# Kernel optimization log

Measured on AMD Instinct MI355X. Metric: run time of the kernel, lower is better.

Reference implementation:

```python
import jax, jax.numpy as jnp
import numpy as np

B, T, C = 2, 2048, 1024
H = 16
D = C // H  # head size 64


def setup_inputs() -> dict:
    key = jax.random.key(0)
    ks = jax.random.split(key, 9)
    s = 0.02
    return {
        "x": jax.random.normal(ks[0], (B, T, C), dtype=jnp.float32),
        "Wq": jax.random.normal(ks[1], (C, C), dtype=jnp.float32) * s,
        "bq": jnp.zeros((C,), dtype=jnp.float32),
        "Wk": jax.random.normal(ks[2], (C, C), dtype=jnp.float32) * s,
        "bk": jnp.zeros((C,), dtype=jnp.float32),
        "Wv": jax.random.normal(ks[3], (C, C), dtype=jnp.float32) * s,
        "bv": jnp.zeros((C,), dtype=jnp.float32),
        "Wo": jax.random.normal(ks[4], (C, C), dtype=jnp.float32) * s,
        "bo": jnp.zeros((C,), dtype=jnp.float32),
    }


def reference(x, Wq, bq, Wk, bk, Wv, bv, Wo, bo):
    b, t, c = x.shape
    scale = 1.0 / jnp.sqrt(jnp.asarray(D, dtype=x.dtype))
    # projections (torch Linear: x @ W.T + b), then split heads -> [B,H,T,D]
    def split_heads(y):
        return y.reshape(b, t, H, D).transpose(0, 2, 1, 3)
    q = split_heads(x @ Wq.T + bq)
    k = split_heads(x @ Wk.T + bk)
    v = split_heads(x @ Wv.T + bv)
    # scores [B,H,T,T], causal mask (triu above diagonal = -inf)
    attn = jnp.einsum("bhqd,bhkd->bhqk", q, k) * scale
    causal = jnp.tril(jnp.ones((t, t), dtype=bool))  # True = keep
    attn = jnp.where(causal[None, None], attn, -jnp.inf)
    attn = jax.nn.softmax(attn, axis=-1)
    # dropout p=0.0 -> identity
    y = jnp.einsum("bhqk,bhkd->bhqd", attn, v)
    y = y.transpose(0, 2, 1, 3).reshape(b, t, c)
    return y @ Wo.T + bo
```

## Files before the change

### kernel.cpp

```cpp
#include <hip/hip_runtime.h>
#include <hip/hip_bf16.h>
#include <stdint.h>
#include <stddef.h>


typedef __bf16 bf16;
typedef __attribute__((ext_vector_type(8))) __bf16 bf16x8;
typedef __attribute__((ext_vector_type(4))) __bf16 bf16x4;
typedef __attribute__((ext_vector_type(4))) float floatx4;

#define MFMA_16x16x32(A, B, C) __builtin_amdgcn_mfma_f32_16x16x32_bf16(A, B, C, 0, 0, 0)

static constexpr int T_SEQ = 2048;
static constexpr int CDIM  = 1024;

__device__ __forceinline__ void gl2lds16(const bf16* g, bf16* l) {
  __builtin_amdgcn_global_load_lds(
      (const __attribute__((address_space(1))) uint32_t*)g,
      (__attribute__((address_space(3))) uint32_t*)l, 16, 0, 0);
}

__global__ __launch_bounds__(256) void convert_kernel(
    const float* __restrict__ x, const float* __restrict__ Wq,
    const float* __restrict__ Wk, const float* __restrict__ Wv,
    const float* __restrict__ Wo,
    bf16* __restrict__ Xb, bf16* __restrict__ Wqkvb, bf16* __restrict__ Wob) {
  size_t i = ((size_t)blockIdx.x * 256 + threadIdx.x) * 4;
  const float* src;
  bf16* dst;
  size_t off;
  if (i < 4194304) {
    src = x; dst = Xb; off = i;
  } else {
    size_t r = i - 4194304;
    int wsel = (int)(r >> 20);
    off = r & 1048575;
    src = (wsel == 0) ? Wq : (wsel == 1) ? Wk : (wsel == 2) ? Wv : Wo;
    dst = (wsel < 3) ? (Wqkvb + ((size_t)wsel << 20)) : Wob;
  }
  float4 v = *(const float4*)(src + off);
  bf16x4 o;
  o[0] = (bf16)v.x; o[1] = (bf16)v.y; o[2] = (bf16)v.z; o[3] = (bf16)v.w;
  *(bf16x4*)(dst + off) = o;
}

__global__ __launch_bounds__(256) void gemm_qkv(
    const bf16* __restrict__ Xb, const bf16* __restrict__ Wqkvb,
    const float* __restrict__ bq, const float* __restrict__ bk,
    const float* __restrict__ bv,
    bf16* __restrict__ Qb, bf16* __restrict__ Kb, bf16* __restrict__ Vtb) {
  __shared__ __align__(16) bf16 smem[12288];
  bf16* As = smem;
  bf16* Bs = smem + 4096;
  bf16* Cs = smem;

  const int bM = blockIdx.x & 63;
  const int bN = blockIdx.x >> 6;
  const int tid = threadIdx.x;
  const int w = tid >> 6, l = tid & 63;
  const int wm = w & 1, wn = w >> 1;
  const int lr = l >> 3, cl = l & 7;
  const int fr = l & 15, q4 = l >> 4;
  const int fc = fr;

  floatx4 acc[2][4];
#pragma unroll
  for (int mi = 0; mi < 2; ++mi)
#pragma unroll
    for (int ni = 0; ni < 4; ++ni)
#pragma unroll
      for (int r = 0; r < 4; ++r) acc[mi][ni][r] = 0.0f;

  for (int k0 = 0; k0 < CDIM; k0 += 64) {
#pragma unroll
    for (int i = 0; i < 2; ++i) {
      int row = i * 32 + w * 8 + lr;
      int cg = cl ^ (row & 7);
      gl2lds16(Xb + (size_t)(bM * 64 + row) * CDIM + k0 + cg * 8,
               As + row * 64 + cl * 8);
    }
#pragma unroll
    for (int i = 0; i < 4; ++i) {
      int row = i * 32 + w * 8 + lr;
      int cg = cl ^ (row & 7);
      gl2lds16(Wqkvb + (size_t)(bN * 128 + row) * CDIM + k0 + cg * 8,
               Bs + row * 64 + cl * 8);
    }
    __syncthreads();
#pragma unroll
    for (int kk = 0; kk < 2; ++kk) {
      const int cgk = kk * 4 + q4;
      bf16x8 af[2], bfr[4];
#pragma unroll
      for (int mi = 0; mi < 2; ++mi) {
        int row = wm * 32 + mi * 16 + fr;
        af[mi] = *(const bf16x8*)(As + row * 64 + (cgk ^ (row & 7)) * 8);
      }
#pragma unroll
      for (int ni = 0; ni < 4; ++ni) {
        int row = wn * 64 + ni * 16 + fr;
        bfr[ni] = *(const bf16x8*)(Bs + row * 64 + (cgk ^ (row & 7)) * 8);
      }
#pragma unroll
      for (int mi = 0; mi < 2; ++mi)
#pragma unroll
        for (int ni = 0; ni < 4; ++ni)
          acc[mi][ni] = MFMA_16x16x32(af[mi], bfr[ni], acc[mi][ni]);
    }
    __syncthreads();
  }

  const int seg = bN >> 3;
  const float QSCALE = 0.125f * 1.44269504089f;
  const float* bp = (seg == 0) ? bq : (seg == 1) ? bk : bv;

#pragma unroll
  for (int ni = 0; ni < 4; ++ni) {
    int jl = wn * 64 + ni * 16 + fc;
    float bias = bp[(bN * 128 + jl) & 1023];
#pragma unroll
    for (int mi = 0; mi < 2; ++mi)
#pragma unroll
      for (int r = 0; r < 4; ++r) {
        int ttl = wm * 32 + mi * 16 + q4 * 4 + r;
        float val = acc[mi][ni][r] + bias;
        if (seg == 0) val *= QSCALE;
        int addr = (seg == 2) ? jl * 72 + ttl : ttl * 136 + jl;
        Cs[addr] = (bf16)val;
      }
  }
  __syncthreads();

  if (seg < 2) {
    bf16* basep = (seg == 0) ? Qb : Kb;
    const int chunk = tid & 15;
    const int rb = (tid >> 4) * 4;
#pragma unroll
    for (int u = 0; u < 4; ++u) {
      int maj = rb + u;
      bf16x8 vdat = *(const bf16x8*)(Cs + maj * 136 + chunk * 8);
      int n = bM * 64 + maj;
      int b = n >> 11, tt = n & 2047;
      int j = bN * 128 + chunk * 8;
      int h = (j >> 6) & 15, d = j & 63;
      *(bf16x8*)(basep + (((size_t)(b * 16 + h) * T_SEQ + tt) << 6) + d) = vdat;
    }
  } else {
    const int chunk = tid & 7;
    const int rb = (tid >> 3) * 4;
#pragma unroll
    for (int u = 0; u < 4; ++u) {
      int maj = rb + u;
      bf16x8 vdat = *(const bf16x8*)(Cs + maj * 72 + chunk * 8);
      int j = bN * 128 + maj;
      int h = (j >> 6) & 15, d = j & 63;
      int n0 = bM * 64 + chunk * 8;
      int b = n0 >> 11, tt0 = n0 & 2047;
      *(bf16x8*)(Vtb + ((size_t)(b * 16 + h) * 64 + d) * T_SEQ + tt0) = vdat;
    }
  }
}

__global__ __launch_bounds__(256) void flash_attn(
    const bf16* __restrict__ Qb, const bf16* __restrict__ Kb,
    const bf16* __restrict__ Vtb, bf16* __restrict__ Ao) {
  __shared__ __align__(16) bf16 Ks[64 * 64];
  __shared__ __align__(16) bf16 Vs[64 * 64];
  __shared__ __align__(16) bf16 Ps[4][16 * 72];

  const int bh = blockIdx.x;
  const int qt = 31 - blockIdx.y;
  const int b = bh >> 4, h = bh & 15;
  const int tid = threadIdx.x;
  const int w = tid >> 6, l = tid & 63;
  const int fc = l & 15, q4 = l >> 4;
  const int lr = l >> 3, cl = l & 7;

  const bf16* Qg = Qb + (size_t)bh * T_SEQ * 64;
  const bf16* Kg = Kb + (size_t)bh * T_SEQ * 64;
  const bf16* Vg = Vtb + (size_t)bh * 64 * T_SEQ;

  const int qrow = qt * 64 + w * 16 + fc;
  bf16x8 qf[2];
  qf[0] = *(const bf16x8*)(Qg + (size_t)qrow * 64 + q4 * 8);
  qf[1] = *(const bf16x8*)(Qg + (size_t)qrow * 64 + 32 + q4 * 8);

  bf16x8 ones;
#pragma unroll
  for (int i = 0; i < 8; ++i) ones[i] = (bf16)1.0f;

  floatx4 o[4];
  floatx4 lacc;
#pragma unroll
  for (int ds = 0; ds < 4; ++ds)
#pragma unroll
    for (int r = 0; r < 4; ++r) o[ds][r] = 0.0f;
#pragma unroll
  for (int r = 0; r < 4; ++r) lacc[r] = 0.0f;

  for (int kv = 0; kv <= qt; ++kv) {
    const int kvbase = kv * 64;
#pragma unroll
    for (int i = 0; i < 2; ++i) {
      int row = i * 32 + w * 8 + lr;
      int cg = cl ^ (row & 7);
      gl2lds16(Kg + (size_t)(kvbase + row) * 64 + cg * 8, Ks + row * 64 + cl * 8);
      gl2lds16(Vg + (size_t)row * T_SEQ + kvbase + cg * 8, Vs + row * 64 + cl * 8);
    }
    __syncthreads();

    floatx4 s[4];
#pragma unroll
    for (int ni = 0; ni < 4; ++ni)
#pragma unroll
      for (int r = 0; r < 4; ++r) s[ni][r] = 0.0f;
#pragma unroll
    for (int kk = 0; kk < 2; ++kk) {
      const int cgk = kk * 4 + q4;
#pragma unroll
      for (int ni = 0; ni < 4; ++ni) {
        int row = ni * 16 + fc;
        bf16x8 kf = *(const bf16x8*)(Ks + row * 64 + (cgk ^ (row & 7)) * 8);
        s[ni] = MFMA_16x16x32(qf[kk], kf, s[ni]);
      }
    }

    if (kv == qt) {
      int qc = w * 16 + q4 * 4;
#pragma unroll
      for (int ni = 0; ni < 4; ++ni)
#pragma unroll
        for (int r = 0; r < 4; ++r) {
          int kc = ni * 16 + fc;
          float p = (kc > qc + r) ? 0.0f : __builtin_amdgcn_exp2f(s[ni][r]);
          Ps[w][(q4 * 4 + r) * 72 + ni * 16 + fc] = (bf16)p;
        }
    } else {
#pragma unroll
      for (int ni = 0; ni < 4; ++ni)
#pragma unroll
        for (int r = 0; r < 4; ++r)
          Ps[w][(q4 * 4 + r) * 72 + ni * 16 + fc] =
              (bf16)__builtin_amdgcn_exp2f(s[ni][r]);
    }

#pragma unroll
    for (int kk = 0; kk < 2; ++kk) {
      bf16x8 pf = *(const bf16x8*)(&Ps[w][fc * 72 + kk * 32 + q4 * 8]);
      const int cgk = kk * 4 + q4;
#pragma unroll
      for (int ds = 0; ds < 4; ++ds) {
        int row = ds * 16 + fc;
        bf16x8 vf = *(const bf16x8*)(Vs + row * 64 + (cgk ^ (row & 7)) * 8);
        o[ds] = MFMA_16x16x32(pf, vf, o[ds]);
      }
      lacc = MFMA_16x16x32(pf, ones, lacc);
    }
    __syncthreads();
  }

  float inv[4];
#pragma unroll
  for (int r = 0; r < 4; ++r) inv[r] = __builtin_amdgcn_rcpf(lacc[r]);
#pragma unroll
  for (int ds = 0; ds < 4; ++ds)
#pragma unroll
    for (int r = 0; r < 4; ++r) {
      int tt = qt * 64 + w * 16 + q4 * 4 + r;
      int col = h * 64 + ds * 16 + fc;
      Ao[((size_t)(b * T_SEQ + tt) << 10) + col] = (bf16)(o[ds][r] * inv[r]);
    }
}

__global__ __launch_bounds__(256) void gemm_out(
    const bf16* __restrict__ Ab, const bf16* __restrict__ Wob,
    const float* __restrict__ bo, float* __restrict__ Y) {
  __shared__ __align__(16) bf16 As[64 * 64];
  __shared__ __align__(16) bf16 Bs[64 * 64];
  const int bM = blockIdx.x & 63;
  const int bN = blockIdx.x >> 6;
  const int tid = threadIdx.x;
  const int w = tid >> 6, l = tid & 63;
  const int wm = w & 1, wn = w >> 1;
  const int lr = l >> 3, cl = l & 7;
  const int fr = l & 15, q4 = l >> 4;
  const int fc = fr;

  floatx4 acc[2][2];
#pragma unroll
  for (int mi = 0; mi < 2; ++mi)
#pragma unroll
    for (int ni = 0; ni < 2; ++ni)
#pragma unroll
      for (int r = 0; r < 4; ++r) acc[mi][ni][r] = 0.0f;

  for (int k0 = 0; k0 < CDIM; k0 += 64) {
#pragma unroll
    for (int i = 0; i < 2; ++i) {
      int row = i * 32 + w * 8 + lr;
      int cg = cl ^ (row & 7);
      gl2lds16(Ab + (size_t)(bM * 64 + row) * CDIM + k0 + cg * 8,
               As + row * 64 + cl * 8);
      gl2lds16(Wob + (size_t)(bN * 64 + row) * CDIM + k0 + cg * 8,
               Bs + row * 64 + cl * 8);
    }
    __syncthreads();
#pragma unroll
    for (int kk = 0; kk < 2; ++kk) {
      const int cgk = kk * 4 + q4;
      bf16x8 af[2], bfr[2];
#pragma unroll
      for (int mi = 0; mi < 2; ++mi) {
        int row = wm * 32 + mi * 16 + fr;
        af[mi] = *(const bf16x8*)(As + row * 64 + (cgk ^ (row & 7)) * 8);
      }
#pragma unroll
      for (int ni = 0; ni < 2; ++ni) {
        int row = wn * 32 + ni * 16 + fr;
        bfr[ni] = *(const bf16x8*)(Bs + row * 64 + (cgk ^ (row & 7)) * 8);
      }
#pragma unroll
      for (int mi = 0; mi < 2; ++mi)
#pragma unroll
        for (int ni = 0; ni < 2; ++ni)
          acc[mi][ni] = MFMA_16x16x32(af[mi], bfr[ni], acc[mi][ni]);
    }
    __syncthreads();
  }

#pragma unroll
  for (int ni = 0; ni < 2; ++ni) {
    int j = bN * 64 + wn * 32 + ni * 16 + fc;
    float bias = bo[j];
#pragma unroll
    for (int mi = 0; mi < 2; ++mi)
#pragma unroll
      for (int r = 0; r < 4; ++r) {
        int n = bM * 64 + wm * 32 + mi * 16 + q4 * 4 + r;
        Y[(size_t)n * CDIM + j] = acc[mi][ni][r] + bias;
      }
  }
}

extern "C" void kernel_launch(void* const* d_in, const int* in_sizes, int n_in,
                              void* d_out, int out_size, void* d_ws, size_t ws_size,
                              hipStream_t stream) {
  const float* x  = (const float*)d_in[0];
  const float* Wq = (const float*)d_in[1];
  const float* bq = (const float*)d_in[2];
  const float* Wk = (const float*)d_in[3];
  const float* bk = (const float*)d_in[4];
  const float* Wv = (const float*)d_in[5];
  const float* bv = (const float*)d_in[6];
  const float* Wo = (const float*)d_in[7];
  const float* bo = (const float*)d_in[8];
  float* Y = (float*)d_out;

  char* ws = (char*)d_ws;
  const size_t MB = 1024 * 1024;
  bf16* Xb    = (bf16*)(ws + 0);
  bf16* Wqkvb = (bf16*)(ws + 8 * MB);
  bf16* Wob   = (bf16*)(ws + 14 * MB);
  bf16* Qb    = (bf16*)(ws + 16 * MB);
  bf16* Kb    = (bf16*)(ws + 24 * MB);
  bf16* Vtb   = (bf16*)(ws + 32 * MB);
  bf16* Ao    = Xb;

  convert_kernel<<<8192, 256, 0, stream>>>(x, Wq, Wk, Wv, Wo, Xb, Wqkvb, Wob);
  gemm_qkv<<<64 * 24, 256, 0, stream>>>(Xb, Wqkvb, bq, bk, bv, Qb, Kb, Vtb);
  flash_attn<<<dim3(32, 32), 256, 0, stream>>>(Qb, Kb, Vtb, Ao);
  gemm_out<<<64 * 16, 256, 0, stream>>>(Ao, Wob, bo, Y);
}
```

Before: 182.4 us.

## Split attention KV loop across two blocks with atomic accumulation and double-buffered LDS

Each query tile's KV iterations are split by parity between two blocks, which doubles the grid and evens out causal load imbalance. Partial unnormalized outputs and row sums are atomically added into fp32 buffers that the convert kernel zeroes first, and a new normalize kernel divides and converts to bf16. K/V staging is double-buffered in LDS, so the next tile's loads overlap the current tile's compute, and one barrier per iteration is removed. The cost is extra fp32 atomic traffic, a 16 MB accumulator, and an additional kernel launch.

```diff
diff --git a/kernel.cpp b/kernel.cpp
--- a/kernel.cpp
+++ b/kernel.cpp
@@ -24,8 +24,16 @@
     const float* __restrict__ x, const float* __restrict__ Wq,
     const float* __restrict__ Wk, const float* __restrict__ Wv,
     const float* __restrict__ Wo,
-    bf16* __restrict__ Xb, bf16* __restrict__ Wqkvb, bf16* __restrict__ Wob) {
+    bf16* __restrict__ Xb, bf16* __restrict__ Wqkvb, bf16* __restrict__ Wob,
+    float* __restrict__ Oacc, float* __restrict__ Lacc) {
   size_t i = ((size_t)blockIdx.x * 256 + threadIdx.x) * 4;
+  if (i >= 8388608) {
+    size_t r = i - 8388608;
+    float4 z = make_float4(0.f, 0.f, 0.f, 0.f);
+    if (r < 4194304) *(float4*)(Oacc + r) = z;
+    else             *(float4*)(Lacc + (r - 4194304)) = z;
+    return;
+  }
   const float* src;
   bf16* dst;
   size_t off;
@@ -163,13 +171,18 @@
 
 __global__ __launch_bounds__(256) void flash_attn(
     const bf16* __restrict__ Qb, const bf16* __restrict__ Kb,
-    const bf16* __restrict__ Vtb, bf16* __restrict__ Ao) {
-  __shared__ __align__(16) bf16 Ks[64 * 64];
-  __shared__ __align__(16) bf16 Vs[64 * 64];
+    const bf16* __restrict__ Vtb, float* __restrict__ Oacc,
+    float* __restrict__ Lacc) {
+  __shared__ __align__(16) bf16 Ks[2 * 64 * 64];
+  __shared__ __align__(16) bf16 Vs[2 * 64 * 64];
   __shared__ __align__(16) bf16 Ps[4][16 * 72];
 
   const int bh = blockIdx.x;
-  const int qt = 31 - blockIdx.y;
+  const int qt = 31 - (blockIdx.y >> 1);
+  const int half = blockIdx.y & 1;
+  const int n = (qt >= half) ? ((qt - half) >> 1) + 1 : 0;
+  if (n == 0) return;
+
   const int b = bh >> 4, h = bh & 15;
   const int tid = threadIdx.x;
   const int w = tid >> 6, l = tid & 63;
@@ -198,16 +211,26 @@
 #pragma unroll
   for (int r = 0; r < 4; ++r) lacc[r] = 0.0f;
 
-  for (int kv = 0; kv <= qt; ++kv) {
-    const int kvbase = kv * 64;
-#pragma unroll
-    for (int i = 0; i < 2; ++i) {
-      int row = i * 32 + w * 8 + lr;
+  auto stage = [&](int pb, int kvb) {
+#pragma unroll
+    for (int i2 = 0; i2 < 2; ++i2) {
+      int row = i2 * 32 + w * 8 + lr;
       int cg = cl ^ (row & 7);
-      gl2lds16(Kg + (size_t)(kvbase + row) * 64 + cg * 8, Ks + row * 64 + cl * 8);
-      gl2lds16(Vg + (size_t)row * T_SEQ + kvbase + cg * 8, Vs + row * 64 + cl * 8);
-    }
+      gl2lds16(Kg + (size_t)(kvb + row) * 64 + cg * 8,
+               Ks + pb * 4096 + row * 64 + cl * 8);
+      gl2lds16(Vg + (size_t)row * T_SEQ + kvb + cg * 8,
+               Vs + pb * 4096 + row * 64 + cl * 8);
+    }
+  };
+
+  stage(0, half * 64);
+  int p = 0;
+  for (int i = 0; i < n; ++i) {
     __syncthreads();
+    if (i + 1 < n) stage(p ^ 1, (half + 2 * (i + 1)) * 64);
+    const int kv = half + 2 * i;
+    const bf16* Ksp = Ks + p * 4096;
+    const bf16* Vsp = Vs + p * 4096;
 
     floatx4 s[4];
 #pragma unroll
@@ -220,7 +243,7 @@
 #pragma unroll
       for (int ni = 0; ni < 4; ++ni) {
         int row = ni * 16 + fc;
-        bf16x8 kf = *(const bf16x8*)(Ks + row * 64 + (cgk ^ (row & 7)) * 8);
+        bf16x8 kf = *(const bf16x8*)(Ksp + row * 64 + (cgk ^ (row & 7)) * 8);
         s[ni] = MFMA_16x16x32(qf[kk], kf, s[ni]);
       }
     }
@@ -232,8 +255,8 @@
 #pragma unroll
         for (int r = 0; r < 4; ++r) {
           int kc = ni * 16 + fc;
-          float p = (kc > qc + r) ? 0.0f : __builtin_amdgcn_exp2f(s[ni][r]);
-          Ps[w][(q4 * 4 + r) * 72 + ni * 16 + fc] = (bf16)p;
+          float pv = (kc > qc + r) ? 0.0f : __builtin_amdgcn_exp2f(s[ni][r]);
+          Ps[w][(q4 * 4 + r) * 72 + ni * 16 + fc] = (bf16)pv;
         }
     } else {
 #pragma unroll
@@ -251,25 +274,45 @@
 #pragma unroll
       for (int ds = 0; ds < 4; ++ds) {
         int row = ds * 16 + fc;
-        bf16x8 vf = *(const bf16x8*)(Vs + row * 64 + (cgk ^ (row & 7)) * 8);
+        bf16x8 vf = *(const bf16x8*)(Vsp + row * 64 + (cgk ^ (row & 7)) * 8);
         o[ds] = MFMA_16x16x32(pf, vf, o[ds]);
       }
       lacc = MFMA_16x16x32(pf, ones, lacc);
     }
-    __syncthreads();
-  }
-
-  float inv[4];
-#pragma unroll
-  for (int r = 0; r < 4; ++r) inv[r] = __builtin_amdgcn_rcpf(lacc[r]);
+    p ^= 1;
+  }
+
 #pragma unroll
   for (int ds = 0; ds < 4; ++ds)
 #pragma unroll
     for (int r = 0; r < 4; ++r) {
       int tt = qt * 64 + w * 16 + q4 * 4 + r;
-      int col = h * 64 + ds * 16 + fc;
-      Ao[((size_t)(b * T_SEQ + tt) << 10) + col] = (bf16)(o[ds][r] * inv[r]);
-    }
+      atomicAdd(Oacc + (((size_t)(b * T_SEQ + tt)) << 10) + h * 64 + ds * 16 + fc,
+                o[ds][r]);
+    }
+  if (fc == 0) {
+#pragma unroll
+    for (int r = 0; r < 4; ++r) {
+      int tt = qt * 64 + w * 16 + q4 * 4 + r;
+      atomicAdd(Lacc + bh * T_SEQ + tt, lacc[r]);
+    }
+  }
+}
+
+__global__ __launch_bounds__(256) void normalize_kernel(
+    const float* __restrict__ Oacc, const float* __restrict__ Lacc,
+    bf16* __restrict__ Ao) {
+  int gid = (blockIdx.x * 256 + threadIdx.x) * 4;
+  int row = gid >> 10;
+  int col = gid & 1023;
+  int b = row >> 11, tt = row & 2047, h = col >> 6;
+  float lv = Lacc[((b << 4) + h) * T_SEQ + tt];
+  float inv = __builtin_amdgcn_rcpf(lv);
+  float4 ov = *(const float4*)(Oacc + gid);
+  bf16x4 r;
+  r[0] = (bf16)(ov.x * inv); r[1] = (bf16)(ov.y * inv);
+  r[2] = (bf16)(ov.z * inv); r[3] = (bf16)(ov.w * inv);
+  *(bf16x4*)(Ao + gid) = r;
 }
 
 __global__ __launch_bounds__(256) void gemm_out(
@@ -358,16 +401,20 @@
 
   char* ws = (char*)d_ws;
   const size_t MB = 1024 * 1024;
-  bf16* Xb    = (bf16*)(ws + 0);
-  bf16* Wqkvb = (bf16*)(ws + 8 * MB);
-  bf16* Wob   = (bf16*)(ws + 14 * MB);
-  bf16* Qb    = (bf16*)(ws + 16 * MB);
-  bf16* Kb    = (bf16*)(ws + 24 * MB);
-  bf16* Vtb   = (bf16*)(ws + 32 * MB);
-  bf16* Ao    = Xb;
-
-  convert_kernel<<<8192, 256, 0, stream>>>(x, Wq, Wk, Wv, Wo, Xb, Wqkvb, Wob);
+  bf16*  Xb    = (bf16*)(ws + 0);
+  bf16*  Wqkvb = (bf16*)(ws + 8 * MB);
+  bf16*  Wob   = (bf16*)(ws + 14 * MB);
+  bf16*  Qb    = (bf16*)(ws + 16 * MB);
+  bf16*  Kb    = (bf16*)(ws + 24 * MB);
+  bf16*  Vtb   = (bf16*)(ws + 32 * MB);
+  float* Oacc  = (float*)(ws + 40 * MB);
+  float* Lacc  = (float*)(ws + 56 * MB);
+  bf16*  Ao    = Xb;
+
+  convert_kernel<<<12352, 256, 0, stream>>>(x, Wq, Wk, Wv, Wo, Xb, Wqkvb, Wob,
+                                            Oacc, Lacc);
   gemm_qkv<<<64 * 24, 256, 0, stream>>>(Xb, Wqkvb, bq, bk, bv, Qb, Kb, Vtb);
-  flash_attn<<<dim3(32, 32), 256, 0, stream>>>(Qb, Kb, Vtb, Ao);
+  flash_attn<<<dim3(32, 64), 256, 0, stream>>>(Qb, Kb, Vtb, Oacc, Lacc);
+  normalize_kernel<<<4096, 256, 0, stream>>>(Oacc, Lacc, Ao);
   gemm_out<<<64 * 16, 256, 0, stream>>>(Ao, Wob, bo, Y);
 }
```

After: 196.9 us. 8.0% more time.

## Double-buffer K/V tiles in flash attention to overlap loads with compute

Applied to the files above, without the earlier changes.

The K and V shared-memory tiles are doubled into ping-pong buffers. The next KV tile's async global-to-LDS load is issued right after the top-of-loop barrier, then the current tile is processed, and the trailing barrier is removed. The aim is to hide global load latency behind the QK and PV MFMA work. The cost is twice the LDS for K/V, which can lower occupancy. The overlap may also be lost if the compiler inserts a full vmcnt wait before the LDS reads.

```diff
diff --git a/kernel.cpp b/kernel.cpp
--- a/kernel.cpp
+++ b/kernel.cpp
@@ -164,8 +164,8 @@
 __global__ __launch_bounds__(256) void flash_attn(
     const bf16* __restrict__ Qb, const bf16* __restrict__ Kb,
     const bf16* __restrict__ Vtb, bf16* __restrict__ Ao) {
-  __shared__ __align__(16) bf16 Ks[64 * 64];
-  __shared__ __align__(16) bf16 Vs[64 * 64];
+  __shared__ __align__(16) bf16 Ks[2 * 64 * 64];
+  __shared__ __align__(16) bf16 Vs[2 * 64 * 64];
   __shared__ __align__(16) bf16 Ps[4][16 * 72];
 
   const int bh = blockIdx.x;
@@ -198,16 +198,25 @@
 #pragma unroll
   for (int r = 0; r < 4; ++r) lacc[r] = 0.0f;
 
+  auto stage = [&](int pb, int kvb) {
+#pragma unroll
+    for (int i2 = 0; i2 < 2; ++i2) {
+      int row = i2 * 32 + w * 8 + lr;
+      int cg = cl ^ (row & 7);
+      gl2lds16(Kg + (size_t)(kvb + row) * 64 + cg * 8,
+               Ks + pb * 4096 + row * 64 + cl * 8);
+      gl2lds16(Vg + (size_t)row * T_SEQ + kvb + cg * 8,
+               Vs + pb * 4096 + row * 64 + cl * 8);
+    }
+  };
+
+  stage(0, 0);
+  int p = 0;
   for (int kv = 0; kv <= qt; ++kv) {
-    const int kvbase = kv * 64;
-#pragma unroll
-    for (int i = 0; i < 2; ++i) {
-      int row = i * 32 + w * 8 + lr;
-      int cg = cl ^ (row & 7);
-      gl2lds16(Kg + (size_t)(kvbase + row) * 64 + cg * 8, Ks + row * 64 + cl * 8);
-      gl2lds16(Vg + (size_t)row * T_SEQ + kvbase + cg * 8, Vs + row * 64 + cl * 8);
-    }
-    __syncthreads();
+    __syncthreads();
+    if (kv < qt) stage(p ^ 1, (kv + 1) * 64);
+    const bf16* Ksp = Ks + p * 4096;
+    const bf16* Vsp = Vs + p * 4096;
 
     floatx4 s[4];
 #pragma unroll
@@ -220,7 +229,7 @@
 #pragma unroll
       for (int ni = 0; ni < 4; ++ni) {
         int row = ni * 16 + fc;
-        bf16x8 kf = *(const bf16x8*)(Ks + row * 64 + (cgk ^ (row & 7)) * 8);
+        bf16x8 kf = *(const bf16x8*)(Ksp + row * 64 + (cgk ^ (row & 7)) * 8);
         s[ni] = MFMA_16x16x32(qf[kk], kf, s[ni]);
       }
     }
@@ -232,8 +241,8 @@
 #pragma unroll
         for (int r = 0; r < 4; ++r) {
           int kc = ni * 16 + fc;
-          float p = (kc > qc + r) ? 0.0f : __builtin_amdgcn_exp2f(s[ni][r]);
-          Ps[w][(q4 * 4 + r) * 72 + ni * 16 + fc] = (bf16)p;
+          float pv = (kc > qc + r) ? 0.0f : __builtin_amdgcn_exp2f(s[ni][r]);
+          Ps[w][(q4 * 4 + r) * 72 + ni * 16 + fc] = (bf16)pv;
         }
     } else {
 #pragma unroll
@@ -251,12 +260,12 @@
 #pragma unroll
       for (int ds = 0; ds < 4; ++ds) {
         int row = ds * 16 + fc;
-        bf16x8 vf = *(const bf16x8*)(Vs + row * 64 + (cgk ^ (row & 7)) * 8);
+        bf16x8 vf = *(const bf16x8*)(Vsp + row * 64 + (cgk ^ (row & 7)) * 8);
         o[ds] = MFMA_16x16x32(pf, vf, o[ds]);
       }
       lacc = MFMA_16x16x32(pf, ones, lacc);
     }
-    __syncthreads();
+    p ^= 1;
   }
 
   float inv[4];
```

Result: no change. 184.9 us (+1.4%).
